# Kernel tuning notes

Hardware: AMD Instinct MI355X
Metric: run time of the kernel (lower is better)

## Reference

```python
import jax, jax.numpy as jnp
import numpy as np

HIDDEN = 128
BSZ, C, Q = 8, 512, 64


def setup_inputs() -> dict:
    key = jax.random.key(0)
    k1, k2, k3, k4 = jax.random.split(key, 4)
    h = jax.random.normal(k1, (BSZ, C, HIDDEN), dtype=jnp.float32)
    u = jax.random.normal(k2, (BSZ, Q, HIDDEN), dtype=jnp.float32)
    # torch Linear stores weight as (out, in); xavier-uniform-like init
    lim1 = float(np.sqrt(6.0 / (3 * HIDDEN + HIDDEN)))
    w1 = jax.random.uniform(k3, (HIDDEN, 3 * HIDDEN), jnp.float32, -lim1, lim1)
    b1 = jnp.zeros((HIDDEN,), jnp.float32)
    lim2 = float(np.sqrt(6.0 / (HIDDEN + 1)))
    w2 = jax.random.uniform(k4, (1, HIDDEN), jnp.float32, -lim2, lim2)
    b2 = jnp.zeros((1,), jnp.float32)
    return {"h": h, "u": u, "w1": w1, "b1": b1, "w2": w2, "b2": b2}


def reference(h, u, w1, b1, w2, b2):
    # Decompose l1 weight into blocks acting on [h2, u2, h2*u2] so the
    # (bsz, C, Q, 3*hidden) concat tensor is never materialized.
    hid = h.shape[-1]
    w_h, w_u, w_hu = w1[:, :hid], w1[:, hid:2 * hid], w1[:, 2 * hid:]
    h_proj = jnp.einsum('bcd,kd->bck', h, w_h)          # (b, C, hidden)
    u_proj = jnp.einsum('bqd,kd->bqk', u, w_u)          # (b, Q, hidden)
    hu_proj = jnp.einsum('bcd,bqd,kd->bcqk', h, u, w_hu)  # (b, C, Q, hidden)
    l1 = jax.nn.relu(h_proj[:, :, None, :] + u_proj[:, None, :, :] + hu_proj + b1)
    l2 = jax.nn.relu(jnp.einsum('bcqk,ok->bcqo', l1, w2) + b2)
    out = jnp.squeeze(l2, axis=-1)  # (b, C, Q)
    if out.ndim == 2:  # bsz == 1 case in original
        out = out[None]
    return out
```

## Files before the change

kernel.cpp:

```cpp
#include <hip/hip_runtime.h>
#include <hip/hip_bf16.h>

typedef __bf16 bf16;
typedef __bf16 bf16x4 __attribute__((ext_vector_type(4)));
typedef __bf16 bf16x8 __attribute__((ext_vector_type(8)));
typedef float  f32x4  __attribute__((ext_vector_type(4)));

#define HID   128
#define BSZ   8
#define CDIM  512
#define QDIM  64
#define LDH   136

__global__ __launch_bounds__(256, 2)
void sim_kernel(const float* __restrict__ hptr,
                const float* __restrict__ uptr,
                const float* __restrict__ w1,
                const float* __restrict__ b1,
                const float* __restrict__ w2,
                const float* __restrict__ b2,
                float* __restrict__ out)
{
    __shared__ bf16  weff[HID * LDH];
    __shared__ float ush[HID];
    __shared__ float bias_sh[HID];
    __shared__ float w2sh[HID];

    const int t  = threadIdx.x;
    const int bi = blockIdx.x >> 6;
    const int qi = blockIdx.x & 63;

    const float* uvec = uptr + (bi * QDIM + qi) * HID;

    if (t < HID) {
        ush[t]  = uvec[t];
        w2sh[t] = w2[t];
    }
    __syncthreads();

    {
        const int k     = t >> 1;
        const int dbase = (t & 1) * 64;
        const float* wrow = w1 + k * 384;
        #pragma unroll
        for (int j = 0; j < 16; ++j) {
            const int d = dbase + j * 4;
            float4 wh  = *(const float4*)(wrow + d);
            float4 whu = *(const float4*)(wrow + 256 + d);
            bf16x4 o;
            o[0] = (bf16)(wh.x + ush[d + 0] * whu.x);
            o[1] = (bf16)(wh.y + ush[d + 1] * whu.y);
            o[2] = (bf16)(wh.z + ush[d + 2] * whu.z);
            o[3] = (bf16)(wh.w + ush[d + 3] * whu.w);
            *(bf16x4*)&weff[k * LDH + d] = o;
        }
    }
    if (t < HID) {
        const float* wrow = w1 + t * 384 + 128;
        float acc = 0.f;
        #pragma unroll 8
        for (int d = 0; d < 128; d += 4) {
            float4 wu = *(const float4*)(wrow + d);
            acc += wu.x * ush[d] + wu.y * ush[d + 1] + wu.z * ush[d + 2] + wu.w * ush[d + 3];
        }
        bias_sh[t] = b1[t] + acc;
    }
    __syncthreads();

    const int lane = t & 63;
    const int wv   = t >> 6;
    const int col  = lane & 15;
    const int quad = lane >> 4;

    bf16x8 bfrag[4][8];
    #pragma unroll
    for (int ks = 0; ks < 4; ++ks)
        #pragma unroll
        for (int n = 0; n < 8; ++n)
            bfrag[ks][n] = *(const bf16x8*)&weff[(n * 16 + col) * LDH + ks * 32 + quad * 8];

    float bias_l[8], w2_l[8];
    #pragma unroll
    for (int n = 0; n < 8; ++n) {
        bias_l[n] = bias_sh[n * 16 + col];
        w2_l[n]   = w2sh[n * 16 + col];
    }
    const float b2v = b2[0];

    const float* hbase = hptr + bi * (CDIM * HID);
    float*       obase = out + (bi * CDIM) * QDIM + qi;

    #pragma unroll 2
    for (int rt = 0; rt < 8; ++rt) {
        const int c0 = wv * 128 + rt * 16;
        const float* arow = hbase + (c0 + col) * HID;

        f32x4 acc[8];
        #pragma unroll
        for (int n = 0; n < 8; ++n) acc[n] = (f32x4){0.f, 0.f, 0.f, 0.f};

        #pragma unroll
        for (int ks = 0; ks < 4; ++ks) {
            const float* ap = arow + ks * 32 + quad * 8;
            float4 v0 = *(const float4*)(ap);
            float4 v1 = *(const float4*)(ap + 4);
            bf16x8 a;
            a[0] = (bf16)v0.x; a[1] = (bf16)v0.y; a[2] = (bf16)v0.z; a[3] = (bf16)v0.w;
            a[4] = (bf16)v1.x; a[5] = (bf16)v1.y; a[6] = (bf16)v1.z; a[7] = (bf16)v1.w;
            #pragma unroll
            for (int n = 0; n < 8; ++n)
                acc[n] = __builtin_amdgcn_mfma_f32_16x16x32_bf16(a, bfrag[ks][n], acc[n], 0, 0, 0);
        }

        float s0 = 0.f, s1 = 0.f, s2 = 0.f, s3 = 0.f;
        #pragma unroll
        for (int n = 0; n < 8; ++n) {
            const float bl = bias_l[n], wl = w2_l[n];
            s0 += fmaxf(acc[n][0] + bl, 0.f) * wl;
            s1 += fmaxf(acc[n][1] + bl, 0.f) * wl;
            s2 += fmaxf(acc[n][2] + bl, 0.f) * wl;
            s3 += fmaxf(acc[n][3] + bl, 0.f) * wl;
        }
        #pragma unroll
        for (int off = 1; off < 16; off <<= 1) {
            s0 += __shfl_xor(s0, off, 64);
            s1 += __shfl_xor(s1, off, 64);
            s2 += __shfl_xor(s2, off, 64);
            s3 += __shfl_xor(s3, off, 64);
        }
        if (col < 4) {
            const float sv = col == 0 ? s0 : col == 1 ? s1 : col == 2 ? s2 : s3;
            const int crow = c0 + quad * 4 + col;
            obase[crow * QDIM] = fmaxf(sv + b2v, 0.f);
        }
    }
}

extern "C" void kernel_launch(void* const* d_in, const int* in_sizes, int n_in,
                              void* d_out, int out_size, void* d_ws, size_t ws_size,
                              hipStream_t stream) {
    const float* h  = (const float*)d_in[0];
    const float* u  = (const float*)d_in[1];
    const float* w1 = (const float*)d_in[2];
    const float* b1 = (const float*)d_in[3];
    const float* w2 = (const float*)d_in[4];
    const float* b2 = (const float*)d_in[5];
    float* out = (float*)d_out;

    sim_kernel<<<dim3(BSZ * QDIM), dim3(256), 0, stream>>>(h, u, w1, b1, w2, b2, out);
}
```

Baseline: 96.51 us.

## Swap MFMA operand roles so hidden dim lies along rows, cutting reduction shuffles

```diff
diff --git a/kernel.cpp b/kernel.cpp
--- a/kernel.cpp
+++ b/kernel.cpp
@@ -12,7 +12,7 @@
 #define QDIM  64
 #define LDH   136
 
-__global__ __launch_bounds__(256, 2)
+__global__ __launch_bounds__(256) __attribute__((amdgpu_waves_per_eu(2, 2)))
 void sim_kernel(const float* __restrict__ hptr,
                 const float* __restrict__ uptr,
                 const float* __restrict__ w1,
@@ -21,14 +21,14 @@
                 const float* __restrict__ b2,
                 float* __restrict__ out)
 {
-    __shared__ bf16  weff[HID * LDH];
-    __shared__ float ush[HID];
-    __shared__ float bias_sh[HID];
-    __shared__ float w2sh[HID];
+    __shared__ __align__(16) bf16  weff[HID * LDH];
+    __shared__ __align__(16) float ush[HID];
+    __shared__ __align__(16) float bias_sh[HID];
+    __shared__ __align__(16) float w2sh[HID];
 
     const int t  = threadIdx.x;
-    const int bi = blockIdx.x >> 6;
-    const int qi = blockIdx.x & 63;
+    const int bi = blockIdx.x & 7;
+    const int qi = blockIdx.x >> 3;
 
     const float* uvec = uptr + (bi * QDIM + qi) * HID;
 
@@ -72,67 +72,56 @@
     const int col  = lane & 15;
     const int quad = lane >> 4;
 
-    bf16x8 bfrag[4][8];
+    bf16x8 afrag[4][8];
     #pragma unroll
     for (int ks = 0; ks < 4; ++ks)
         #pragma unroll
-        for (int n = 0; n < 8; ++n)
-            bfrag[ks][n] = *(const bf16x8*)&weff[(n * 16 + col) * LDH + ks * 32 + quad * 8];
+        for (int mt = 0; mt < 8; ++mt)
+            afrag[ks][mt] = *(const bf16x8*)&weff[(mt * 16 + col) * LDH + ks * 32 + quad * 8];
 
-    float bias_l[8], w2_l[8];
+    f32x4 bias4[8], w24[8];
     #pragma unroll
-    for (int n = 0; n < 8; ++n) {
-        bias_l[n] = bias_sh[n * 16 + col];
-        w2_l[n]   = w2sh[n * 16 + col];
+    for (int mt = 0; mt < 8; ++mt) {
+        bias4[mt] = *(const f32x4*)&bias_sh[mt * 16 + quad * 4];
+        w24[mt]   = *(const f32x4*)&w2sh[mt * 16 + quad * 4];
     }
     const float b2v = b2[0];
 
-    const float* hbase = hptr + bi * (CDIM * HID);
+    const float* hb    = hptr + bi * (CDIM * HID);
     float*       obase = out + (bi * CDIM) * QDIM + qi;
 
-    #pragma unroll 2
-    for (int rt = 0; rt < 8; ++rt) {
-        const int c0 = wv * 128 + rt * 16;
-        const float* arow = hbase + (c0 + col) * HID;
+    for (int chunk = 0; chunk < 8; ++chunk) {
+        const int c0 = wv * 128 + chunk * 16;
+        const float* brow = hb + (c0 + col) * HID + quad * 8;
 
         f32x4 acc[8];
         #pragma unroll
-        for (int n = 0; n < 8; ++n) acc[n] = (f32x4){0.f, 0.f, 0.f, 0.f};
+        for (int mt = 0; mt < 8; ++mt) acc[mt] = bias4[mt];
 
         #pragma unroll
         for (int ks = 0; ks < 4; ++ks) {
-            const float* ap = arow + ks * 32 + quad * 8;
-            float4 v0 = *(const float4*)(ap);
-            float4 v1 = *(const float4*)(ap + 4);
-            bf16x8 a;
-            a[0] = (bf16)v0.x; a[1] = (bf16)v0.y; a[2] = (bf16)v0.z; a[3] = (bf16)v0.w;
-            a[4] = (bf16)v1.x; a[5] = (bf16)v1.y; a[6] = (bf16)v1.z; a[7] = (bf16)v1.w;
+            float4 v0 = *(const float4*)(brow + ks * 32);
+            float4 v1 = *(const float4*)(brow + ks * 32 + 4);
+            bf16x8 b;
+            b[0] = (bf16)v0.x; b[1] = (bf16)v0.y; b[2] = (bf16)v0.z; b[3] = (bf16)v0.w;
+            b[4] = (bf16)v1.x; b[5] = (bf16)v1.y; b[6] = (bf16)v1.z; b[7] = (bf16)v1.w;
             #pragma unroll
-            for (int n = 0; n < 8; ++n)
-                acc[n] = __builtin_amdgcn_mfma_f32_16x16x32_bf16(a, bfrag[ks][n], acc[n], 0, 0, 0);
+            for (int mt = 0; mt < 8; ++mt)
+                acc[mt] = __builtin_amdgcn_mfma_f32_16x16x32_bf16(afrag[ks][mt], b, acc[mt], 0, 0, 0);
         }
 
-        float s0 = 0.f, s1 = 0.f, s2 = 0.f, s3 = 0.f;
+        float s = 0.f;
         #pragma unroll
-        for (int n = 0; n < 8; ++n) {
-            const float bl = bias_l[n], wl = w2_l[n];
-            s0 += fmaxf(acc[n][0] + bl, 0.f) * wl;
-            s1 += fmaxf(acc[n][1] + bl, 0.f) * wl;
-            s2 += fmaxf(acc[n][2] + bl, 0.f) * wl;
-            s3 += fmaxf(acc[n][3] + bl, 0.f) * wl;
+        for (int mt = 0; mt < 8; ++mt) {
+            s += fmaxf(acc[mt][0], 0.f) * w24[mt][0];
+            s += fmaxf(acc[mt][1], 0.f) * w24[mt][1];
+            s += fmaxf(acc[mt][2], 0.f) * w24[mt][2];
+            s += fmaxf(acc[mt][3], 0.f) * w24[mt][3];
         }
-        #pragma unroll
-        for (int off = 1; off < 16; off <<= 1) {
-            s0 += __shfl_xor(s0, off, 64);
-            s1 += __shfl_xor(s1, off, 64);
-            s2 += __shfl_xor(s2, off, 64);
-            s3 += __shfl_xor(s3, off, 64);
-        }
-        if (col < 4) {
-            const float sv = col == 0 ? s0 : col == 1 ? s1 : col == 2 ? s2 : s3;
-            const int crow = c0 + quad * 4 + col;
-            obase[crow * QDIM] = fmaxf(sv + b2v, 0.f);
-        }
+        s += __shfl_xor(s, 16, 64);
+        s += __shfl_xor(s, 32, 64);
+        if (lane < 16)
+            obase[(c0 + col) * QDIM] = fmaxf(s + b2v, 0.f);
     }
 }
 
```

Result: faster. 91.74 us (-4.9%).
